# Kernel optimization log

Hardware: AMD Instinct MI355X
Metric: run time of the kernel (lower is better)

Reference implementation:

```python
import jax, jax.numpy as jnp
import numpy as np

B, S, H, E, V = 128, 128, 1024, 512, 32000  # batch, src_len, hidden (enc==dec), embed, vocab


def setup_inputs() -> dict:
    key = jax.random.key(0)
    ks = jax.random.split(key, 16)
    g = lambda k, shape: jax.random.normal(k, shape, dtype=jnp.float32) * 0.02
    return {
        "target_lang": jax.random.randint(ks[0], (B,), 0, V),
        "decoder_hidden": jax.random.normal(ks[1], (B, H), dtype=jnp.float32),
        "encoder_output": jax.random.normal(ks[2], (S, B, 2 * H), dtype=jnp.float32),
        "emb": g(ks[3], (V, E)),
        "W1": g(ks[4], (H, 3 * H)),       # attention fc1 (in = 2H enc + H dec)
        "b1": jnp.zeros((H,), jnp.float32),
        "W2": g(ks[5], (1, H)),            # attention fc2
        "b2": jnp.zeros((1,), jnp.float32),
        "Wih": g(ks[6], (3 * H, 2 * H + E)),  # GRU input weights [r;z;n]
        "Whh": g(ks[7], (3 * H, H)),          # GRU hidden weights [r;z;n]
        "bih": jnp.zeros((3 * H,), jnp.float32),
        "bhh": jnp.zeros((3 * H,), jnp.float32),
        "Wout": g(ks[8], (V, E + 3 * H)),     # output projection
        "bout": jnp.zeros((V,), jnp.float32),
    }


def reference(target_lang, decoder_hidden, encoder_output, emb, W1, b1, W2, b2,
              Wih, Whh, bih, bhh, Wout, bout):
    # Embedding lookup (dropout is identity in eval mode)
    embeds = emb[target_lang]                                   # [B, E]

    # --- Additive (Bahdanau) attention ---
    enc = jnp.transpose(encoder_output, (1, 0, 2))              # [B, S, 2H]
    hid = jnp.broadcast_to(decoder_hidden[:, None, :], (B, S, H))
    concat = jnp.concatenate([enc, hid], axis=-1)               # [B, S, 3H]
    energy = jnp.tanh(concat @ W1.T + b1)                       # [B, S, H]
    scores = energy @ W2.T + b2                                 # [B, S, 1]
    alpha = jax.nn.softmax(scores, axis=1)[..., 0]              # [B, S]
    a = jnp.einsum('bs,bsd->bd', alpha, enc)                    # [B, 2H]

    # --- single-step GRU ---
    x = jnp.concatenate([embeds, a], axis=-1)                   # [B, E+2H]
    gx = x @ Wih.T + bih                                        # [B, 3H]
    gh = decoder_hidden @ Whh.T + bhh                           # [B, 3H]
    xr, xz, xn = jnp.split(gx, 3, axis=-1)
    hr, hz, hn = jnp.split(gh, 3, axis=-1)
    r = jax.nn.sigmoid(xr + hr)
    z = jax.nn.sigmoid(xz + hz)
    n = jnp.tanh(xn + r * hn)
    h_new = (1.0 - z) * n + z * decoder_hidden                  # [B, H]

    # --- output projection ---
    c1 = jnp.concatenate([h_new, a, embeds], axis=-1)           # [B, H+2H+E]
    pred = c1 @ Wout.T + bout                                   # [B, V]
    return pred, h_new
```

## Files before the change

### kernel.cpp

```cpp
#include <hip/hip_runtime.h>
#include <hip/hip_bf16.h>
#include <cmath>


#define DEVINL __device__ __forceinline__

typedef __attribute__((ext_vector_type(8))) __bf16 bf16x8;
typedef __attribute__((ext_vector_type(4))) float f32x4;

DEVINL unsigned short f2bf(float f) {
    unsigned u = __builtin_bit_cast(unsigned, f);
    unsigned r = (u + 0x7FFFu + ((u >> 16) & 1u)) >> 16;
    return (unsigned short)r;
}

DEVINL float fast_tanh(float x) {
    x = fminf(15.0f, fmaxf(-15.0f, x));
    float e = __expf(2.0f * x);
    return (e - 1.0f) / (e + 1.0f);
}

DEVINL float sigmoidf_(float x) { return 1.0f / (1.0f + __expf(-x)); }


__global__ void embed_gather_k(const int* __restrict__ tl,
                               const float* __restrict__ emb,
                               unsigned short* __restrict__ xbuf,
                               unsigned short* __restrict__ c1) {
    int id = blockIdx.x * blockDim.x + threadIdx.x;
    if (id >= 128 * 512) return;
    int b = id >> 9, e = id & 511;
    unsigned short v = f2bf(emb[(size_t)tl[b] * 512 + e]);
    xbuf[b * 2560 + e] = v;
    c1[b * 3584 + 3072 + e] = v;
}

template<int BN, int ADT, int EPI>
__global__ void __launch_bounds__(256)
gemm_tpl(const void* __restrict__ Av, int lda,
         const float* __restrict__ W, int ldw,
         const float* __restrict__ bias,
         float* __restrict__ C, int ldc, int K,
         const float* __restrict__ hproj,
         const float* __restrict__ W2v,
         float* __restrict__ scores) {
    constexpr int JF = BN / 32;
    constexpr int A_F4 = 8;
    constexpr int A_U4 = 4;
    constexpr int W_F4 = BN / 16;

    __shared__ unsigned short As[2][128 * 64];
    __shared__ unsigned short Bs[2][BN * 64];

    const int t = threadIdx.x;
    const int m0 = (EPI == 1) ? blockIdx.x * 128 : 0;
    const int n0 = (EPI == 1) ? blockIdx.y * BN : blockIdx.x * BN;
    const int wid = t >> 6, lane = t & 63;
    const int wm = (wid & 1) * 64;
    const int wn = (wid >> 1) * (JF * 16);
    const int quad = lane >> 4, l16 = lane & 15;

    const float* Af = (const float*)Av;
    const unsigned short* Ab = (const unsigned short*)Av;

    f32x4 acc[4][JF] = {};
    float4 pa[ADT == 0 ? A_F4 : 1];
    uint4 pab[ADT == 1 ? A_U4 : 1];
    float4 pw[W_F4];

    auto issue = [&](int k0) {
        if constexpr (ADT == 0) {
            for (int i = 0; i < A_F4; ++i) {
                int idx = t + i * 256, row = idx >> 4, c4 = (idx & 15) * 4;
                pa[i] = *(const float4*)(Af + (size_t)(m0 + row) * lda + k0 + c4);
            }
        } else {
            for (int i = 0; i < A_U4; ++i) {
                int idx = t + i * 256, row = idx >> 3, c8 = (idx & 7) * 8;
                pab[i] = *(const uint4*)(Ab + (size_t)(m0 + row) * lda + k0 + c8);
            }
        }
        for (int i = 0; i < W_F4; ++i) {
            int idx = t + i * 256, row = idx >> 4, c4 = (idx & 15) * 4;
            pw[i] = *(const float4*)(W + (size_t)(n0 + row) * ldw + k0 + c4);
        }
    };
    auto commit = [&](int buf) {
        if constexpr (ADT == 0) {
            for (int i = 0; i < A_F4; ++i) {
                int idx = t + i * 256, row = idx >> 4, c4 = (idx & 15) * 4;
                ushort4 s;
                s.x = f2bf(pa[i].x); s.y = f2bf(pa[i].y);
                s.z = f2bf(pa[i].z); s.w = f2bf(pa[i].w);
                *(ushort4*)&As[buf][row * 64 + c4] = s;
            }
        } else {
            for (int i = 0; i < A_U4; ++i) {
                int idx = t + i * 256, row = idx >> 3, c8 = (idx & 7) * 8;
                *(uint4*)&As[buf][row * 64 + c8] = pab[i];
            }
        }
        for (int i = 0; i < W_F4; ++i) {
            int idx = t + i * 256, row = idx >> 4, c4 = (idx & 15) * 4;
            ushort4 s;
            s.x = f2bf(pw[i].x); s.y = f2bf(pw[i].y);
            s.z = f2bf(pw[i].z); s.w = f2bf(pw[i].w);
            *(ushort4*)&Bs[buf][row * 64 + c4] = s;
        }
    };

    issue(0);
    commit(0);
    __syncthreads();

    int buf = 0;
    for (int k0 = 0; k0 < K; k0 += 64) {
        bool nxt = (k0 + 64) < K;
        if (nxt) issue(k0 + 64);
        for (int kk = 0; kk < 64; kk += 32) {
            bf16x8 af[4], bfr[JF];
            for (int i = 0; i < 4; ++i)
                af[i] = *(const bf16x8*)&As[buf][(wm + i * 16 + l16) * 64 + kk + quad * 8];
            for (int j = 0; j < JF; ++j)
                bfr[j] = *(const bf16x8*)&Bs[buf][(wn + j * 16 + l16) * 64 + kk + quad * 8];
            for (int i = 0; i < 4; ++i)
                for (int j = 0; j < JF; ++j)
                    acc[i][j] = __builtin_amdgcn_mfma_f32_16x16x32_bf16(af[i], bfr[j], acc[i][j], 0, 0, 0);
        }
        if (nxt) {
            commit(buf ^ 1);
            __syncthreads();
            buf ^= 1;
        }
    }

    if constexpr (EPI == 0) {
        for (int i = 0; i < 4; ++i)
            for (int j = 0; j < JF; ++j) {
                int colg = n0 + wn + j * 16 + l16;
                float bv = bias[colg];
                for (int r = 0; r < 4; ++r) {
                    int rowg = wm + i * 16 + quad * 4 + r;
                    C[(size_t)rowg * ldc + colg] = acc[i][j][r] + bv;
                }
            }
    } else {
        for (int i = 0; i < 4; ++i)
            for (int r = 0; r < 4; ++r) {
                int rowg = m0 + wm + i * 16 + quad * 4 + r;
                int b = rowg & 127;
                float partial = 0.0f;
                for (int j = 0; j < JF; ++j) {
                    int colg = n0 + wn + j * 16 + l16;
                    float v = fast_tanh(acc[i][j][r] + hproj[b * 1024 + colg]);
                    partial += v * W2v[colg];
                }
                partial += __shfl_xor(partial, 1, 64);
                partial += __shfl_xor(partial, 2, 64);
                partial += __shfl_xor(partial, 4, 64);
                partial += __shfl_xor(partial, 8, 64);
                if (l16 == 0) atomicAdd(&scores[rowg], partial);
            }
    }
}

__global__ void __launch_bounds__(256)
attn_combine_k(const float* __restrict__ scores,
               const float* __restrict__ enc,
               unsigned short* __restrict__ xbuf,
               unsigned short* __restrict__ c1) {
    const int b = blockIdx.x;
    const int t = threadIdx.x;
    __shared__ float alpha[128];
    __shared__ float red[256];

    float sc = (t < 128) ? scores[t * 128 + b] : -1e30f;
    red[t] = sc;
    __syncthreads();
    for (int s = 128; s > 0; s >>= 1) {
        if (t < s) red[t] = fmaxf(red[t], red[t + s]);
        __syncthreads();
    }
    float mx = red[0];
    __syncthreads();
    float e = (t < 128) ? __expf(sc - mx) : 0.0f;
    red[t] = e;
    __syncthreads();
    for (int s = 128; s > 0; s >>= 1) {
        if (t < s) red[t] += red[t + s];
        __syncthreads();
    }
    float denom = red[0];
    if (t < 128) alpha[t] = e / denom;
    __syncthreads();

    float acc[8] = {};
    for (int s = 0; s < 128; ++s) {
        float al = alpha[s];
        const float* erow = enc + ((size_t)(s * 128 + b)) * 2048;
        for (int i = 0; i < 8; ++i)
            acc[i] += al * erow[t + i * 256];
    }
    for (int i = 0; i < 8; ++i) {
        int d = t + i * 256;
        unsigned short v = f2bf(acc[i]);
        xbuf[b * 2560 + 512 + d] = v;
        c1[b * 3584 + 1024 + d] = v;
    }
}

__global__ void gru_gates_k(const float* __restrict__ gx,
                            const float* __restrict__ gh,
                            const float* __restrict__ dh,
                            float* __restrict__ out_h,
                            unsigned short* __restrict__ c1) {
    int id = blockIdx.x * blockDim.x + threadIdx.x;
    if (id >= 128 * 1024) return;
    int b = id >> 10, h = id & 1023;
    const float* gxb = gx + b * 3072;
    const float* ghb = gh + b * 3072;
    float r = sigmoidf_(gxb[h] + ghb[h]);
    float z = sigmoidf_(gxb[1024 + h] + ghb[1024 + h]);
    float n = fast_tanh(gxb[2048 + h] + r * ghb[2048 + h]);
    float hprev = dh[b * 1024 + h];
    float hnew = (1.0f - z) * n + z * hprev;
    out_h[b * 1024 + h] = hnew;
    c1[b * 3584 + h] = f2bf(hnew);
}

extern "C" void kernel_launch(void* const* d_in, const int* in_sizes, int n_in,
                              void* d_out, int out_size, void* d_ws, size_t ws_size,
                              hipStream_t stream) {
    const int* tl = (const int*)d_in[0];
    const float* dh = (const float*)d_in[1];
    const float* enc = (const float*)d_in[2];
    const float* emb = (const float*)d_in[3];
    const float* W1 = (const float*)d_in[4];
    const float* b1 = (const float*)d_in[5];
    const float* W2 = (const float*)d_in[6];
    const float* Wih = (const float*)d_in[8];
    const float* Whh = (const float*)d_in[9];
    const float* bih = (const float*)d_in[10];
    const float* bhh = (const float*)d_in[11];
    const float* Wout = (const float*)d_in[12];
    const float* bout = (const float*)d_in[13];

    float* out_pred = (float*)d_out;
    float* out_h = out_pred + (size_t)128 * 32000;

    float* ws = (float*)d_ws;
    float* hproj = ws;
    float* scores = ws + 131072;
    unsigned short* xbuf = (unsigned short*)(ws + 147456);
    unsigned short* c1 = (unsigned short*)(ws + 311296);
    float* gx = ws + 540672;
    float* gh = ws + 933888;

    embed_gather_k<<<256, 256, 0, stream>>>(tl, emb, xbuf, c1);

    gemm_tpl<64, 0, 0><<<16, 256, 0, stream>>>(
        dh, 1024, W1 + 2048, 3072, b1, hproj, 1024, 1024, nullptr, nullptr, nullptr);

    gemm_tpl<64, 0, 0><<<48, 256, 0, stream>>>(
        dh, 1024, Whh, 1024, bhh, gh, 3072, 1024, nullptr, nullptr, nullptr);

    hipMemsetAsync(scores, 0, 16384 * sizeof(float), stream);

    dim3 gs(128, 8);
    gemm_tpl<128, 0, 1><<<gs, 256, 0, stream>>>(
        enc, 2048, W1, 3072, nullptr, nullptr, 0, 2048, hproj, W2, scores);

    attn_combine_k<<<128, 256, 0, stream>>>(scores, enc, xbuf, c1);

    gemm_tpl<64, 1, 0><<<48, 256, 0, stream>>>(
        xbuf, 2560, Wih, 2560, bih, gx, 3072, 2560, nullptr, nullptr, nullptr);

    gru_gates_k<<<512, 256, 0, stream>>>(gx, gh, dh, out_h, c1);

    gemm_tpl<64, 1, 0><<<500, 256, 0, stream>>>(
        c1, 3584, Wout, 3584, bout, out_pred, 32000, 3584, nullptr, nullptr, nullptr);
}
```

Measured before the change: 1.197 ms.

## Pre-convert weights to bf16, swizzle LDS tiles, reorder attention grid, split combine

Adds a kernel that converts W1, Whh and Wih to bf16 in scratch space inside the output buffer, so the GEMMs load bf16 weights instead of converting fp32 in every tile. The GEMM loads in 8-element chunks and XOR-swizzles the LDS layout to cut bank conflicts. The attention GEMM grid is transposed so blocks sharing an encoder tile run next to each other. The attention combine is split over two blocks per batch row with float4 loads. The extra conversion passes add their own memory traffic, and the scratch reuse of out_pred depends on the final GEMM overwriting it afterwards.

New measurement: 1.265 ms. 1.06x slower.

```diff
diff --git a/kernel.cpp b/kernel.cpp
--- a/kernel.cpp
+++ b/kernel.cpp
@@ -1,5 +1,4 @@
 #include <hip/hip_runtime.h>
-#include <hip/hip_bf16.h>
 #include <cmath>
 
 
@@ -7,6 +6,7 @@
 
 typedef __attribute__((ext_vector_type(8))) __bf16 bf16x8;
 typedef __attribute__((ext_vector_type(4))) float f32x4;
+typedef __attribute__((ext_vector_type(8))) unsigned short u16x8;
 
 DEVINL unsigned short f2bf(float f) {
     unsigned u = __builtin_bit_cast(unsigned, f);
@@ -22,6 +22,18 @@
 
 DEVINL float sigmoidf_(float x) { return 1.0f / (1.0f + __expf(-x)); }
 
+__global__ void cvt_bf16_k(const float* __restrict__ in,
+                           unsigned short* __restrict__ out, int n8) {
+    int id = blockIdx.x * blockDim.x + threadIdx.x;
+    if (id >= n8) return;
+    const float* p = in + (size_t)id * 8;
+    float4 a = *(const float4*)p;
+    float4 c = *(const float4*)(p + 4);
+    u16x8 s;
+    s[0] = f2bf(a.x); s[1] = f2bf(a.y); s[2] = f2bf(a.z); s[3] = f2bf(a.w);
+    s[4] = f2bf(c.x); s[5] = f2bf(c.y); s[6] = f2bf(c.z); s[7] = f2bf(c.w);
+    *(u16x8*)(out + (size_t)id * 8) = s;
+}
 
 __global__ void embed_gather_k(const int* __restrict__ tl,
                                const float* __restrict__ emb,
@@ -35,26 +47,25 @@
     c1[b * 3584 + 3072 + e] = v;
 }
 
-template<int BN, int ADT, int EPI>
+template<int BN, int ADT, int WDT, int EPI>
 __global__ void __launch_bounds__(256)
 gemm_tpl(const void* __restrict__ Av, int lda,
-         const float* __restrict__ W, int ldw,
+         const void* __restrict__ Wv, int ldw,
          const float* __restrict__ bias,
          float* __restrict__ C, int ldc, int K,
          const float* __restrict__ hproj,
          const float* __restrict__ W2v,
          float* __restrict__ scores) {
     constexpr int JF = BN / 32;
-    constexpr int A_F4 = 8;
-    constexpr int A_U4 = 4;
-    constexpr int W_F4 = BN / 16;
+    constexpr int ACH = 4;
+    constexpr int WCH = BN / 32;
 
     __shared__ unsigned short As[2][128 * 64];
     __shared__ unsigned short Bs[2][BN * 64];
 
     const int t = threadIdx.x;
-    const int m0 = (EPI == 1) ? blockIdx.x * 128 : 0;
-    const int n0 = (EPI == 1) ? blockIdx.y * BN : blockIdx.x * BN;
+    const int m0 = (EPI == 1) ? blockIdx.y * 128 : 0;
+    const int n0 = blockIdx.x * BN;
     const int wid = t >> 6, lane = t & 63;
     const int wm = (wid & 1) * 64;
     const int wn = (wid >> 1) * (JF * 16);
@@ -62,50 +73,65 @@
 
     const float* Af = (const float*)Av;
     const unsigned short* Ab = (const unsigned short*)Av;
+    const float* Wf = (const float*)Wv;
+    const unsigned short* Wb = (const unsigned short*)Wv;
 
     f32x4 acc[4][JF] = {};
-    float4 pa[ADT == 0 ? A_F4 : 1];
-    uint4 pab[ADT == 1 ? A_U4 : 1];
-    float4 pw[W_F4];
+    float4 paf[ADT == 0 ? 2 * ACH : 1];
+    uint4 pab[ADT == 1 ? ACH : 1];
+    float4 pwf[WDT == 0 ? 2 * WCH : 1];
+    uint4 pwb[WDT == 1 ? WCH : 1];
 
     auto issue = [&](int k0) {
-        if constexpr (ADT == 0) {
-            for (int i = 0; i < A_F4; ++i) {
-                int idx = t + i * 256, row = idx >> 4, c4 = (idx & 15) * 4;
-                pa[i] = *(const float4*)(Af + (size_t)(m0 + row) * lda + k0 + c4);
-            }
-        } else {
-            for (int i = 0; i < A_U4; ++i) {
-                int idx = t + i * 256, row = idx >> 3, c8 = (idx & 7) * 8;
+        for (int i = 0; i < ACH; ++i) {
+            int idx = t + i * 256, row = idx >> 3, c8 = (idx & 7) * 8;
+            if constexpr (ADT == 0) {
+                const float* p = Af + (size_t)(m0 + row) * lda + k0 + c8;
+                paf[2 * i] = *(const float4*)p;
+                paf[2 * i + 1] = *(const float4*)(p + 4);
+            } else {
                 pab[i] = *(const uint4*)(Ab + (size_t)(m0 + row) * lda + k0 + c8);
             }
         }
-        for (int i = 0; i < W_F4; ++i) {
-            int idx = t + i * 256, row = idx >> 4, c4 = (idx & 15) * 4;
-            pw[i] = *(const float4*)(W + (size_t)(n0 + row) * ldw + k0 + c4);
+        for (int i = 0; i < WCH; ++i) {
+            int idx = t + i * 256, row = idx >> 3, c8 = (idx & 7) * 8;
+            if constexpr (WDT == 0) {
+                const float* p = Wf + (size_t)(n0 + row) * ldw + k0 + c8;
+                pwf[2 * i] = *(const float4*)p;
+                pwf[2 * i + 1] = *(const float4*)(p + 4);
+            } else {
+                pwb[i] = *(const uint4*)(Wb + (size_t)(n0 + row) * ldw + k0 + c8);
+            }
         }
     };
     auto commit = [&](int buf) {
-        if constexpr (ADT == 0) {
-            for (int i = 0; i < A_F4; ++i) {
-                int idx = t + i * 256, row = idx >> 4, c4 = (idx & 15) * 4;
-                ushort4 s;
-                s.x = f2bf(pa[i].x); s.y = f2bf(pa[i].y);
-                s.z = f2bf(pa[i].z); s.w = f2bf(pa[i].w);
-                *(ushort4*)&As[buf][row * 64 + c4] = s;
-            }
-        } else {
-            for (int i = 0; i < A_U4; ++i) {
-                int idx = t + i * 256, row = idx >> 3, c8 = (idx & 7) * 8;
-                *(uint4*)&As[buf][row * 64 + c8] = pab[i];
-            }
-        }
-        for (int i = 0; i < W_F4; ++i) {
-            int idx = t + i * 256, row = idx >> 4, c4 = (idx & 15) * 4;
-            ushort4 s;
-            s.x = f2bf(pw[i].x); s.y = f2bf(pw[i].y);
-            s.z = f2bf(pw[i].z); s.w = f2bf(pw[i].w);
-            *(ushort4*)&Bs[buf][row * 64 + c4] = s;
+        for (int i = 0; i < ACH; ++i) {
+            int idx = t + i * 256, row = idx >> 3, c = idx & 7;
+            unsigned short* dst = &As[buf][row * 64 + ((c ^ (row & 7)) << 3)];
+            if constexpr (ADT == 0) {
+                u16x8 s;
+                s[0] = f2bf(paf[2 * i].x); s[1] = f2bf(paf[2 * i].y);
+                s[2] = f2bf(paf[2 * i].z); s[3] = f2bf(paf[2 * i].w);
+                s[4] = f2bf(paf[2 * i + 1].x); s[5] = f2bf(paf[2 * i + 1].y);
+                s[6] = f2bf(paf[2 * i + 1].z); s[7] = f2bf(paf[2 * i + 1].w);
+                *(u16x8*)dst = s;
+            } else {
+                *(uint4*)dst = pab[i];
+            }
+        }
+        for (int i = 0; i < WCH; ++i) {
+            int idx = t + i * 256, row = idx >> 3, c = idx & 7;
+            unsigned short* dst = &Bs[buf][row * 64 + ((c ^ (row & 7)) << 3)];
+            if constexpr (WDT == 0) {
+                u16x8 s;
+                s[0] = f2bf(pwf[2 * i].x); s[1] = f2bf(pwf[2 * i].y);
+                s[2] = f2bf(pwf[2 * i].z); s[3] = f2bf(pwf[2 * i].w);
+                s[4] = f2bf(pwf[2 * i + 1].x); s[5] = f2bf(pwf[2 * i + 1].y);
+                s[6] = f2bf(pwf[2 * i + 1].z); s[7] = f2bf(pwf[2 * i + 1].w);
+                *(u16x8*)dst = s;
+            } else {
+                *(uint4*)dst = pwb[i];
+            }
         }
     };
 
@@ -118,11 +144,16 @@
         bool nxt = (k0 + 64) < K;
         if (nxt) issue(k0 + 64);
         for (int kk = 0; kk < 64; kk += 32) {
+            const int cb = (kk >> 3) + quad;
             bf16x8 af[4], bfr[JF];
-            for (int i = 0; i < 4; ++i)
-                af[i] = *(const bf16x8*)&As[buf][(wm + i * 16 + l16) * 64 + kk + quad * 8];
-            for (int j = 0; j < JF; ++j)
-                bfr[j] = *(const bf16x8*)&Bs[buf][(wn + j * 16 + l16) * 64 + kk + quad * 8];
+            for (int i = 0; i < 4; ++i) {
+                int r = wm + i * 16 + l16;
+                af[i] = *(const bf16x8*)&As[buf][r * 64 + ((cb ^ (r & 7)) << 3)];
+            }
+            for (int j = 0; j < JF; ++j) {
+                int rn = wn + j * 16 + l16;
+                bfr[j] = *(const bf16x8*)&Bs[buf][rn * 64 + ((cb ^ (rn & 7)) << 3)];
+            }
             for (int i = 0; i < 4; ++i)
                 for (int j = 0; j < JF; ++j)
                     acc[i][j] = __builtin_amdgcn_mfma_f32_16x16x32_bf16(af[i], bfr[j], acc[i][j], 0, 0, 0);
@@ -169,7 +200,8 @@
                const float* __restrict__ enc,
                unsigned short* __restrict__ xbuf,
                unsigned short* __restrict__ c1) {
-    const int b = blockIdx.x;
+    const int b = blockIdx.x >> 1;
+    const int half = blockIdx.x & 1;
     const int t = threadIdx.x;
     __shared__ float alpha[128];
     __shared__ float red[256];
@@ -190,23 +222,22 @@
         if (t < s) red[t] += red[t + s];
         __syncthreads();
     }
-    float denom = red[0];
-    if (t < 128) alpha[t] = e / denom;
-    __syncthreads();
-
-    float acc[8] = {};
+    if (t < 128) alpha[t] = e / red[0];
+    __syncthreads();
+
+    const int d = half * 1024 + t * 4;
+    const float* ep = enc + (size_t)b * 2048 + d;
+    float ax = 0.f, ay = 0.f, az = 0.f, aw = 0.f;
+#pragma unroll 4
     for (int s = 0; s < 128; ++s) {
         float al = alpha[s];
-        const float* erow = enc + ((size_t)(s * 128 + b)) * 2048;
-        for (int i = 0; i < 8; ++i)
-            acc[i] += al * erow[t + i * 256];
-    }
-    for (int i = 0; i < 8; ++i) {
-        int d = t + i * 256;
-        unsigned short v = f2bf(acc[i]);
-        xbuf[b * 2560 + 512 + d] = v;
-        c1[b * 3584 + 1024 + d] = v;
-    }
+        float4 v = *(const float4*)(ep + (size_t)s * 128 * 2048);
+        ax += al * v.x; ay += al * v.y; az += al * v.z; aw += al * v.w;
+    }
+    ushort4 s4;
+    s4.x = f2bf(ax); s4.y = f2bf(ay); s4.z = f2bf(az); s4.w = f2bf(aw);
+    *(ushort4*)&xbuf[b * 2560 + 512 + d] = s4;
+    *(ushort4*)&c1[b * 3584 + 1024 + d] = s4;
 }
 
 __global__ void gru_gates_k(const float* __restrict__ gx,
@@ -256,27 +287,36 @@
     float* gx = ws + 540672;
     float* gh = ws + 933888;
 
+    unsigned short* w1bf = (unsigned short*)out_pred;
+    unsigned short* whhbf = w1bf + 1024 * 3072;
+    unsigned short* wihbf = (unsigned short*)out_pred;
+
     embed_gather_k<<<256, 256, 0, stream>>>(tl, emb, xbuf, c1);
 
-    gemm_tpl<64, 0, 0><<<16, 256, 0, stream>>>(
-        dh, 1024, W1 + 2048, 3072, b1, hproj, 1024, 1024, nullptr, nullptr, nullptr);
-
-    gemm_tpl<64, 0, 0><<<48, 256, 0, stream>>>(
-        dh, 1024, Whh, 1024, bhh, gh, 3072, 1024, nullptr, nullptr, nullptr);
+    cvt_bf16_k<<<1536, 256, 0, stream>>>(W1, w1bf, 1024 * 3072 / 8);
+    cvt_bf16_k<<<1536, 256, 0, stream>>>(Whh, whhbf, 3072 * 1024 / 8);
+
+    gemm_tpl<64, 0, 1, 0><<<16, 256, 0, stream>>>(
+        dh, 1024, w1bf + 2048, 3072, b1, hproj, 1024, 1024, nullptr, nullptr, nullptr);
+
+    gemm_tpl<64, 0, 1, 0><<<48, 256, 0, stream>>>(
+        dh, 1024, whhbf, 1024, bhh, gh, 3072, 1024, nullptr, nullptr, nullptr);
 
     hipMemsetAsync(scores, 0, 16384 * sizeof(float), stream);
 
-    dim3 gs(128, 8);
-    gemm_tpl<128, 0, 1><<<gs, 256, 0, stream>>>(
-        enc, 2048, W1, 3072, nullptr, nullptr, 0, 2048, hproj, W2, scores);
-
-    attn_combine_k<<<128, 256, 0, stream>>>(scores, enc, xbuf, c1);
-
-    gemm_tpl<64, 1, 0><<<48, 256, 0, stream>>>(
-        xbuf, 2560, Wih, 2560, bih, gx, 3072, 2560, nullptr, nullptr, nullptr);
+    dim3 gs(8, 128);
+    gemm_tpl<128, 0, 1, 1><<<gs, 256, 0, stream>>>(
+        enc, 2048, w1bf, 3072, nullptr, nullptr, 0, 2048, hproj, W2, scores);
+
+    attn_combine_k<<<256, 256, 0, stream>>>(scores, enc, xbuf, c1);
+
+    cvt_bf16_k<<<3840, 256, 0, stream>>>(Wih, wihbf, 3072 * 2560 / 8);
+
+    gemm_tpl<64, 1, 1, 0><<<48, 256, 0, stream>>>(
+        xbuf, 2560, wihbf, 2560, bih, gx, 3072, 2560, nullptr, nullptr, nullptr);
 
     gru_gates_k<<<512, 256, 0, stream>>>(gx, gh, dh, out_h, c1);
 
-    gemm_tpl<64, 1, 0><<<500, 256, 0, stream>>>(
+    gemm_tpl<64, 1, 0, 0><<<500, 256, 0, stream>>>(
         c1, 3584, Wout, 3584, bout, out_pred, 32000, 3584, nullptr, nullptr, nullptr);
 }
```
